# Kernel tuning notes

Hardware: AMD Instinct MI355X
Metric: run time of the kernel (lower is better)

## Reference

```python
import jax, jax.numpy as jnp
import numpy as np

N = 50000      # nodes per graph
E = 600000     # edges per graph
IN_DIM = 512
HID = 128
LAYERS = 2


def setup_inputs() -> dict:
    key = jax.random.key(0)
    ks = jax.random.split(key, 24)
    s = 0.05
    inp = {
        "src_fea": jax.random.normal(ks[0], (N, IN_DIM), jnp.float32),
        "trg_fea": jax.random.normal(ks[1], (N, IN_DIM), jnp.float32),
        "src_row": jax.random.randint(ks[2], (E,), 0, N, jnp.int32),
        "src_col": jax.random.randint(ks[3], (E,), 0, N, jnp.int32),
        "trg_row": jax.random.randint(ks[4], (E,), 0, N, jnp.int32),
        "trg_col": jax.random.randint(ks[5], (E,), 0, N, jnp.int32),
        # fx: Linear(in,hid)+GELU+Linear(hid,hid)+GELU
        "fxW1": jax.random.normal(ks[6], (IN_DIM, HID), jnp.float32) * s,
        "fxb1": jnp.zeros((HID,), jnp.float32),
        "fxW2": jax.random.normal(ks[7], (HID, HID), jnp.float32) * s,
        "fxb2": jnp.zeros((HID,), jnp.float32),
        # edge_att_mlp: Linear(2h,20)+ReLU+Linear(20,10)+ReLU+Linear(10,1)+ReLU
        "eaW1": jax.random.normal(ks[8], (2 * HID, 20), jnp.float32) * s,
        "eab1": jnp.zeros((20,), jnp.float32),
        "eaW2": jax.random.normal(ks[9], (20, 10), jnp.float32) * s,
        "eab2": jnp.zeros((10,), jnp.float32),
        "eaW3": jax.random.normal(ks[10], (10, 1), jnp.float32) * s,
        "eab3": jnp.zeros((1,), jnp.float32),
        # GraphConv (PyG-style, bias=False): out = x@Wroot + agg@Wrel
        "convWroot": jax.random.normal(ks[11], (LAYERS, HID, HID), jnp.float32) * s,
        "convWrel": jax.random.normal(ks[12], (LAYERS, HID, HID), jnp.float32) * s,
    }
    return inp


def _fx(x, W1, b1, W2, b2):
    h = jax.nn.gelu(x @ W1 + b1, approximate=False)
    return jax.nn.gelu(h @ W2 + b2, approximate=False)


def _edge_att(e, eaW1, eab1, eaW2, eab2, eaW3, eab3):
    h = jax.nn.relu(e @ eaW1 + eab1)
    h = jax.nn.relu(h @ eaW2 + eab2)
    h = jax.nn.relu(h @ eaW3 + eab3)
    return jax.nn.sigmoid(h)  # [E,1]


def _graph_conv(x, row, col, ew, Wroot, Wrel):
    # message from source (row) gathered, weighted, aggregated at target (col)
    msg = ew[:, None] * x[row]                                  # [E,h]
    agg = jax.ops.segment_sum(msg, col, num_segments=N)         # [N,h]
    return x @ Wroot + agg @ Wrel


def _branch(x0, row, col, convWroot, convWrel, eaW1, eab1, eaW2, eab2, eaW3, eab3, hard):
    xs, cfds = [], []
    x = x0
    for i in range(LAYERS):
        edge_rep = jnp.concatenate([x[row], x[col]], axis=-1)    # [E,2h]
        att = _edge_att(edge_rep, eaW1, eab1, eaW2, eab2, eaW3, eab3)[:, 0]
        wc = (att + hard) * 0.5
        wo = 1.0 - wc
        x = jax.nn.soft_sign(_graph_conv(x, row, col, wc, convWroot[i], convWrel[i]))
        cfd = jax.nn.soft_sign(_graph_conv(x, row, col, wo, convWroot[i], convWrel[i]))
        xs.append(x)
        cfds.append(cfd)
    return xs, cfds


def reference(src_fea, trg_fea, src_row, src_col, trg_row, trg_col,
              fxW1, fxb1, fxW2, fxb2,
              eaW1, eab1, eaW2, eab2, eaW3, eab3,
              convWroot, convWrel):
    src1 = _fx(src_fea, fxW1, fxb1, fxW2, fxb2)
    trg1 = _fx(trg_fea, fxW1, fxb1, fxW2, fxb2)
    ea = (eaW1, eab1, eaW2, eab2, eaW3, eab3)
    xs_s, cf_s = _branch(src1, src_row, src_col, convWroot, convWrel, *ea, 0.0)
    xs_t, cf_t = _branch(trg1, trg_row, trg_col, convWroot, convWrel, *ea, 0.0)
    # stack: [src1, xs_s..., trg1, xs_t..., cf_s..., cf_t...] -> [2+2*LAYERS+2*LAYERS? no: 10, N, h]
    return jnp.stack([src1] + xs_s + [trg1] + xs_t + cf_s + cf_t, axis=0)
```

## Files before the change

### kernel.cpp

```cpp
#include <hip/hip_runtime.h>
#include <math.h>
#include <stdint.h>


typedef __attribute__((ext_vector_type(8))) short bh8;
typedef __attribute__((ext_vector_type(4))) float f4;

__device__ __forceinline__ float relu_f(float x) { return x > 0.f ? x : 0.f; }

__device__ __forceinline__ unsigned short f2bf(float f) {
    union { float f; unsigned u; } v; v.f = f;
    unsigned r = v.u + 0x7FFF + ((v.u >> 16) & 1);
    return (unsigned short)(r >> 16);
}
__device__ __forceinline__ float bf2f(unsigned short b) {
    union { unsigned u; float f; } v; v.u = ((unsigned)b) << 16;
    return v.f;
}

template<int ACT>
__device__ __forceinline__ float act_fn(float x) {
    if (ACT == 1) return 0.5f * x * (1.f + erff(x * 0.70710678118654752f));
    if (ACT == 2) return x / (1.f + fabsf(x));
    return x;
}

__device__ __forceinline__ void emit_p_phase(short* As, short* Bs,
                                             const short* __restrict__ W56,
                                             short* __restrict__ P,
                                             int row0, int M, int t)
{
    #pragma unroll
    for (int p = 0; p < 4; ++p) {
        int idx = t + 256 * p;
        int r = idx >> 4;
        int c = (idx & 15) * 8;
        *(bh8*)&Bs[r * 136 + c] = *(const bh8*)(W56 + r * 128 + c);
    }
    __syncthreads();
    const int lane = t & 63, w = t >> 6, l15 = lane & 15, l4 = lane >> 4;
    f4 accP[4];
    #pragma unroll
    for (int ni = 0; ni < 4; ++ni) accP[ni] = (f4){0.f, 0.f, 0.f, 0.f};
    #pragma unroll
    for (int kk = 0; kk < 4; ++kk) {
        bh8 a = *(const bh8*)&As[(w * 16 + l15) * 136 + kk * 32 + l4 * 8];
        #pragma unroll
        for (int ni = 0; ni < 4; ++ni) {
            bh8 b = *(const bh8*)&Bs[(ni * 16 + l15) * 136 + kk * 32 + l4 * 8];
            accP[ni] = __builtin_amdgcn_mfma_f32_16x16x32_bf16(a, b, accP[ni], 0, 0, 0);
        }
    }
    #pragma unroll
    for (int ni = 0; ni < 4; ++ni) {
        int col = ni * 16 + l15;
        #pragma unroll
        for (int r = 0; r < 4; ++r) {
            int row = row0 + w * 16 + l4 * 4 + r;
            if (row < M) P[(size_t)row * 64 + col] = (short)f2bf(accP[ni][r]);
        }
    }
}

template<int K, int AF, int ACT, bool BIAS, bool WF32, bool WB16, bool EMITP>
__global__ __launch_bounds__(256, 2)
void mfma_gemm(const void* __restrict__ X0a, const void* __restrict__ X0b,
               const short* __restrict__ W0t, const float* __restrict__ bias,
               float* __restrict__ outfA, short* __restrict__ outbA,
               float* __restrict__ outfB, short* __restrict__ outbB,
               const short* __restrict__ W56,
               short* __restrict__ PA, short* __restrict__ PB, int M)
{
    constexpr int BK  = 64;
    constexpr int LDA = EMITP ? 136 : 72;
    __shared__ short As[64 * LDA];
    __shared__ short Bs[128 * 72];

    const int half = gridDim.x >> 1;
    int bid = blockIdx.x;
    const int g1 = bid >= half;
    bid -= g1 ? half : 0;
    const void* X0v = g1 ? X0b : X0a;
    float* outf = g1 ? outfB : outfA;
    short* outb = g1 ? outbB : outbA;
    short* P    = g1 ? PB : PA;

    const int t    = threadIdx.x;
    const int row0 = bid * 64;
    const int lane = t & 63;
    const int w    = t >> 6;
    const int wr   = w & 1;
    const int wc   = w >> 1;
    const int l15  = lane & 15;
    const int l4   = lane >> 4;

    f4 acc[2][4];
    #pragma unroll
    for (int i = 0; i < 2; ++i)
        #pragma unroll
        for (int j = 0; j < 4; ++j)
            acc[i][j] = (f4){0.f, 0.f, 0.f, 0.f};

    const int ar = t >> 3;
    const int ac = (t & 7) * 8;

    #pragma unroll 1
    for (int k0 = 0; k0 < K; k0 += BK) {
        __syncthreads();
        #pragma unroll
        for (int p = 0; p < 2; ++p) {
            int r    = ar + p * 32;
            int grow = row0 + r;
            bh8 sv = {0, 0, 0, 0, 0, 0, 0, 0};
            if (AF == 0) {
                if (grow < M) {
                    const float* src = (const float*)X0v + (size_t)grow * K + k0 + ac;
                    float4 v0 = *(const float4*)src;
                    float4 v1 = *(const float4*)(src + 4);
                    sv[0] = (short)f2bf(v0.x); sv[1] = (short)f2bf(v0.y);
                    sv[2] = (short)f2bf(v0.z); sv[3] = (short)f2bf(v0.w);
                    sv[4] = (short)f2bf(v1.x); sv[5] = (short)f2bf(v1.y);
                    sv[6] = (short)f2bf(v1.z); sv[7] = (short)f2bf(v1.w);
                }
            } else {
                if (grow < M)
                    sv = *(const bh8*)((const short*)X0v + (size_t)grow * K + k0 + ac);
            }
            *(bh8*)&As[r * LDA + ac] = sv;
        }
        #pragma unroll
        for (int p = 0; p < 4; ++p) {
            int r = ar + p * 32;
            *(bh8*)&Bs[r * 72 + ac] = *(const bh8*)(W0t + (size_t)r * K + k0 + ac);
        }
        __syncthreads();
        #pragma unroll
        for (int kk = 0; kk < 2; ++kk) {
            bh8 a[2], b[4];
            #pragma unroll
            for (int mi = 0; mi < 2; ++mi)
                a[mi] = *(const bh8*)&As[(wr*32 + mi*16 + l15) * LDA + kk*32 + l4*8];
            #pragma unroll
            for (int ni = 0; ni < 4; ++ni)
                b[ni] = *(const bh8*)&Bs[(wc*64 + ni*16 + l15) * 72 + kk*32 + l4*8];
            #pragma unroll
            for (int mi = 0; mi < 2; ++mi)
                #pragma unroll
                for (int ni = 0; ni < 4; ++ni)
                    acc[mi][ni] = __builtin_amdgcn_mfma_f32_16x16x32_bf16(
                        a[mi], b[ni], acc[mi][ni], 0, 0, 0);
        }
    }

    if (EMITP) __syncthreads();
    #pragma unroll
    for (int mi = 0; mi < 2; ++mi) {
        #pragma unroll
        for (int ni = 0; ni < 4; ++ni) {
            int col = wc * 64 + ni * 16 + l15;
            float bv = BIAS ? bias[col] : 0.f;
            #pragma unroll
            for (int r = 0; r < 4; ++r) {
                int rloc = wr * 32 + mi * 16 + l4 * 4 + r;
                int row  = row0 + rloc;
                float v = act_fn<ACT>(acc[mi][ni][r] + bv);
                unsigned short bb = f2bf(v);
                if (row < M) {
                    if (WF32) outf[(size_t)row * 128 + col] = v;
                    if (WB16) outb[(size_t)row * 128 + col] = (short)bb;
                }
                if (EMITP) As[rloc * LDA + col] = (short)bb;
            }
        }
    }
    if (EMITP) emit_p_phase(As, Bs, W56, P, row0, M, t);
}

template<int MODE, bool WB16, bool EMITP>
__global__ __launch_bounds__(256, 2)
void conv_fused(const short* __restrict__ XbA, const short* __restrict__ XbB,
                const int* __restrict__ coffA, const int* __restrict__ coffB,
                const int* __restrict__ crowA, const int* __restrict__ crowB,
                const float* __restrict__ attcA, const float* __restrict__ attcB,
                const short* __restrict__ Wroot, const short* __restrict__ Wrel,
                const short* __restrict__ W56,
                float* __restrict__ outfA, float* __restrict__ outfB,
                short* __restrict__ outbA, short* __restrict__ outbB,
                short* __restrict__ PA, short* __restrict__ PB, int M)
{
    constexpr int LDA = 136;
    __shared__ short As[64 * LDA];
    __shared__ short Bs[128 * 72];

    const int half = gridDim.x >> 1;
    int bid = blockIdx.x;
    const int g1 = bid >= half;
    bid -= g1 ? half : 0;
    const short* Xb   = g1 ? XbB   : XbA;
    const int*   coff = g1 ? coffB : coffA;
    const int*   crow = g1 ? crowB : crowA;
    const float* attc = g1 ? attcB : attcA;
    float* outf = g1 ? outfB : outfA;
    short* outb = g1 ? outbB : outbA;
    short* P    = g1 ? PB : PA;

    const int t    = threadIdx.x;
    const int row0 = bid * 64;
    const int lane = t & 63;
    const int w    = t >> 6;
    const int wr   = w & 1;
    const int wc   = w >> 1;
    const int l15  = lane & 15;
    const int l4   = lane >> 4;

    {
        const int g  = t >> 4;
        const int li = t & 15;
        #pragma unroll 1
        for (int q = 0; q < 4; ++q) {
            int rloc = g * 4 + q;
            int n = row0 + rloc;
            float a8[8] = {0.f, 0.f, 0.f, 0.f, 0.f, 0.f, 0.f, 0.f};
            if (n < M) {
                int p  = coff[n];
                int pe = coff[n + 1];
                for (; p + 7 < pe; p += 8) {
                    float w0 = attc[p],     w1 = attc[p + 1];
                    float w2 = attc[p + 2], w3 = attc[p + 3];
                    float w4 = attc[p + 4], w5 = attc[p + 5];
                    float w6 = attc[p + 6], w7 = attc[p + 7];
                    int r0 = crow[p],     r1 = crow[p + 1];
                    int r2 = crow[p + 2], r3 = crow[p + 3];
                    int r4 = crow[p + 4], r5 = crow[p + 5];
                    int r6 = crow[p + 6], r7 = crow[p + 7];
                    w0 = MODE ? fmaf(-0.5f, w0, 1.f) : 0.5f * w0;
                    w1 = MODE ? fmaf(-0.5f, w1, 1.f) : 0.5f * w1;
                    w2 = MODE ? fmaf(-0.5f, w2, 1.f) : 0.5f * w2;
                    w3 = MODE ? fmaf(-0.5f, w3, 1.f) : 0.5f * w3;
                    w4 = MODE ? fmaf(-0.5f, w4, 1.f) : 0.5f * w4;
                    w5 = MODE ? fmaf(-0.5f, w5, 1.f) : 0.5f * w5;
                    w6 = MODE ? fmaf(-0.5f, w6, 1.f) : 0.5f * w6;
                    w7 = MODE ? fmaf(-0.5f, w7, 1.f) : 0.5f * w7;
                    bh8 v0 = *(const bh8*)&Xb[(size_t)r0 * 128 + li * 8];
                    bh8 v1 = *(const bh8*)&Xb[(size_t)r1 * 128 + li * 8];
                    bh8 v2 = *(const bh8*)&Xb[(size_t)r2 * 128 + li * 8];
                    bh8 v3 = *(const bh8*)&Xb[(size_t)r3 * 128 + li * 8];
                    bh8 v4 = *(const bh8*)&Xb[(size_t)r4 * 128 + li * 8];
                    bh8 v5 = *(const bh8*)&Xb[(size_t)r5 * 128 + li * 8];
                    bh8 v6 = *(const bh8*)&Xb[(size_t)r6 * 128 + li * 8];
                    bh8 v7 = *(const bh8*)&Xb[(size_t)r7 * 128 + li * 8];
                    #pragma unroll
                    for (int j = 0; j < 8; ++j) {
                        a8[j] = fmaf(w0, bf2f((unsigned short)v0[j]), a8[j]);
                        a8[j] = fmaf(w1, bf2f((unsigned short)v1[j]), a8[j]);
                        a8[j] = fmaf(w2, bf2f((unsigned short)v2[j]), a8[j]);
                        a8[j] = fmaf(w3, bf2f((unsigned short)v3[j]), a8[j]);
                        a8[j] = fmaf(w4, bf2f((unsigned short)v4[j]), a8[j]);
                        a8[j] = fmaf(w5, bf2f((unsigned short)v5[j]), a8[j]);
                        a8[j] = fmaf(w6, bf2f((unsigned short)v6[j]), a8[j]);
                        a8[j] = fmaf(w7, bf2f((unsigned short)v7[j]), a8[j]);
                    }
                }
                for (; p + 3 < pe; p += 4) {
                    float w0 = attc[p],     w1 = attc[p + 1];
                    float w2 = attc[p + 2], w3 = attc[p + 3];
                    int r0 = crow[p],     r1 = crow[p + 1];
                    int r2 = crow[p + 2], r3 = crow[p + 3];
                    w0 = MODE ? fmaf(-0.5f, w0, 1.f) : 0.5f * w0;
                    w1 = MODE ? fmaf(-0.5f, w1, 1.f) : 0.5f * w1;
                    w2 = MODE ? fmaf(-0.5f, w2, 1.f) : 0.5f * w2;
                    w3 = MODE ? fmaf(-0.5f, w3, 1.f) : 0.5f * w3;
                    bh8 v0 = *(const bh8*)&Xb[(size_t)r0 * 128 + li * 8];
                    bh8 v1 = *(const bh8*)&Xb[(size_t)r1 * 128 + li * 8];
                    bh8 v2 = *(const bh8*)&Xb[(size_t)r2 * 128 + li * 8];
                    bh8 v3 = *(const bh8*)&Xb[(size_t)r3 * 128 + li * 8];
                    #pragma unroll
                    for (int j = 0; j < 8; ++j) {
                        a8[j] = fmaf(w0, bf2f((unsigned short)v0[j]), a8[j]);
                        a8[j] = fmaf(w1, bf2f((unsigned short)v1[j]), a8[j]);
                        a8[j] = fmaf(w2, bf2f((unsigned short)v2[j]), a8[j]);
                        a8[j] = fmaf(w3, bf2f((unsigned short)v3[j]), a8[j]);
                    }
                }
                for (; p < pe; ++p) {
                    float w0 = attc[p];
                    int   r0 = crow[p];
                    w0 = MODE ? fmaf(-0.5f, w0, 1.f) : 0.5f * w0;
                    bh8 v0 = *(const bh8*)&Xb[(size_t)r0 * 128 + li * 8];
                    #pragma unroll
                    for (int j = 0; j < 8; ++j)
                        a8[j] = fmaf(w0, bf2f((unsigned short)v0[j]), a8[j]);
                }
            }
            bh8 o;
            #pragma unroll
            for (int j = 0; j < 8; ++j) o[j] = (short)f2bf(a8[j]);
            *(bh8*)&As[rloc * LDA + li * 8] = o;
        }
    }
    __syncthreads();

    f4 acc[2][4];
    #pragma unroll
    for (int i = 0; i < 2; ++i)
        #pragma unroll
        for (int j = 0; j < 4; ++j)
            acc[i][j] = (f4){0.f, 0.f, 0.f, 0.f};

    const int ar = t >> 3;
    const int ac = (t & 7) * 8;

    #pragma unroll 1
    for (int k0 = 0; k0 < 128; k0 += 64) {
        if (k0) __syncthreads();
        #pragma unroll
        for (int p = 0; p < 4; ++p) {
            int r = ar + p * 32;
            *(bh8*)&Bs[r * 72 + ac] = *(const bh8*)(Wrel + (size_t)r * 128 + k0 + ac);
        }
        __syncthreads();
        #pragma unroll
        for (int kk = 0; kk < 2; ++kk) {
            bh8 a[2], b[4];
            #pragma unroll
            for (int mi = 0; mi < 2; ++mi)
                a[mi] = *(const bh8*)&As[(wr*32 + mi*16 + l15) * LDA + k0 + kk*32 + l4*8];
            #pragma unroll
            for (int ni = 0; ni < 4; ++ni)
                b[ni] = *(const bh8*)&Bs[(wc*64 + ni*16 + l15) * 72 + kk*32 + l4*8];
            #pragma unroll
            for (int mi = 0; mi < 2; ++mi)
                #pragma unroll
                for (int ni = 0; ni < 4; ++ni)
                    acc[mi][ni] = __builtin_amdgcn_mfma_f32_16x16x32_bf16(
                        a[mi], b[ni], acc[mi][ni], 0, 0, 0);
        }
    }

    #pragma unroll 1
    for (int k0 = 0; k0 < 128; k0 += 64) {
        __syncthreads();
        #pragma unroll
        for (int p = 0; p < 2; ++p) {
            int r    = ar + p * 32;
            int grow = row0 + r;
            bh8 sv = {0, 0, 0, 0, 0, 0, 0, 0};
            if (grow < M)
                sv = *(const bh8*)(Xb + (size_t)grow * 128 + k0 + ac);
            *(bh8*)&As[r * LDA + ac] = sv;
        }
        #pragma unroll
        for (int p = 0; p < 4; ++p) {
            int r = ar + p * 32;
            *(bh8*)&Bs[r * 72 + ac] = *(const bh8*)(Wroot + (size_t)r * 128 + k0 + ac);
        }
        __syncthreads();
        #pragma unroll
        for (int kk = 0; kk < 2; ++kk) {
            bh8 a[2], b[4];
            #pragma unroll
            for (int mi = 0; mi < 2; ++mi)
                a[mi] = *(const bh8*)&As[(wr*32 + mi*16 + l15) * LDA + kk*32 + l4*8];
            #pragma unroll
            for (int ni = 0; ni < 4; ++ni)
                b[ni] = *(const bh8*)&Bs[(wc*64 + ni*16 + l15) * 72 + kk*32 + l4*8];
            #pragma unroll
            for (int mi = 0; mi < 2; ++mi)
                #pragma unroll
                for (int ni = 0; ni < 4; ++ni)
                    acc[mi][ni] = __builtin_amdgcn_mfma_f32_16x16x32_bf16(
                        a[mi], b[ni], acc[mi][ni], 0, 0, 0);
        }
    }

    if (EMITP) __syncthreads();
    #pragma unroll
    for (int mi = 0; mi < 2; ++mi) {
        #pragma unroll
        for (int ni = 0; ni < 4; ++ni) {
            int col = wc * 64 + ni * 16 + l15;
            #pragma unroll
            for (int r = 0; r < 4; ++r) {
                int rloc = wr * 32 + mi * 16 + l4 * 4 + r;
                int row  = row0 + rloc;
                float v = act_fn<2>(acc[mi][ni][r]);
                unsigned short bb = f2bf(v);
                if (row < M) {
                    outf[(size_t)row * 128 + col] = v;
                    if (WB16) outb[(size_t)row * 128 + col] = (short)bb;
                }
                if (EMITP) As[rloc * LDA + col] = (short)bb;
            }
        }
    }
    if (EMITP) emit_p_phase(As, Bs, W56, P, row0, M, t);
}

__global__ void prep_all(const float* __restrict__ eaW1, const float* __restrict__ fxW1,
                         const float* __restrict__ fxW2, const float* __restrict__ convWroot,
                         const float* __restrict__ convWrel,
                         short* __restrict__ w56, short* __restrict__ fxW1t,
                         short* __restrict__ fxW2t, short* __restrict__ wrt,
                         short* __restrict__ wlt)
{
    int i = blockIdx.x * 256 + threadIdx.x;
    if (i < 64 * 128) {
        int j = i >> 7, k = i & 127;
        float v = 0.f;
        if (j < 20)                  v = eaW1[k * 20 + j];
        else if (j >= 32 && j < 52)  v = eaW1[(128 + k) * 20 + (j - 32)];
        w56[i] = (short)f2bf(v);
        return;
    }
    i -= 64 * 128;
    if (i < 512 * 128) {
        int k = i >> 7, n = i & 127;
        fxW1t[(size_t)n * 512 + k] = (short)f2bf(fxW1[i]);
        return;
    }
    i -= 512 * 128;
    if (i < 128 * 128) {
        int k = i >> 7, n = i & 127;
        fxW2t[n * 128 + k] = (short)f2bf(fxW2[i]);
        return;
    }
    i -= 128 * 128;
    if (i < 2 * 128 * 128) {
        int L = i >> 14, r = i & 16383;
        int k = r >> 7, n = r & 127;
        wrt[L * 16384 + n * 128 + k] = (short)f2bf(convWroot[i]);
        return;
    }
    i -= 2 * 128 * 128;
    if (i < 2 * 128 * 128) {
        int L = i >> 14, r = i & 16383;
        int k = r >> 7, n = r & 127;
        wlt[L * 16384 + n * 128 + k] = (short)f2bf(convWrel[i]);
    }
}

__global__ __launch_bounds__(256)
void edge_att_both(const short* __restrict__ PS, const short* __restrict__ PT,
                   const int* __restrict__ rowS, const int* __restrict__ colS,
                   const int* __restrict__ rowT, const int* __restrict__ colT,
                   const int* __restrict__ eposS, const int* __restrict__ eposT,
                   const float* __restrict__ eab1, const float* __restrict__ eaW2,
                   const float* __restrict__ eab2, const float* __restrict__ eaW3,
                   const float* __restrict__ eab3,
                   float* __restrict__ attcS, float* __restrict__ attcT, int E)
{
    __shared__ float w2[200], b2s[10], w3s[10], sb1[20], sb3;
    int t = threadIdx.x;
    if (t < 200) w2[t] = eaW2[t];
    if (t < 20)  sb1[t] = eab1[t];
    if (t < 10)  { b2s[t] = eab2[t]; w3s[t] = eaW3[t]; }
    if (t == 0)  sb3 = eab3[0];
    __syncthreads();

    int idx = blockIdx.x * 256 + t;
    if (idx >= 2 * E) return;
    const int g1 = idx >= E;
    const int e  = idx - (g1 ? E : 0);
    const short* P    = g1 ? PT : PS;
    const int*   row  = g1 ? rowT : rowS;
    const int*   col  = g1 ? colT : colS;
    const int*   epos = g1 ? eposT : eposS;
    float*       attc = g1 ? attcT : attcS;

    int r = row[e], c = col[e];
    const unsigned short* p1 = (const unsigned short*)P + (size_t)r * 64;
    const unsigned short* p2 = (const unsigned short*)P + (size_t)c * 64 + 32;

    bh8 a0 = *(const bh8*)&p1[0];
    bh8 a1 = *(const bh8*)&p1[8];
    ushort4 a2 = *(const ushort4*)&p1[16];
    bh8 b0 = *(const bh8*)&p2[0];
    bh8 b1 = *(const bh8*)&p2[8];
    ushort4 b2 = *(const ushort4*)&p2[16];

    float h1[20];
    #pragma unroll
    for (int j = 0; j < 8; ++j)
        h1[j] = relu_f(bf2f((unsigned short)a0[j]) + bf2f((unsigned short)b0[j]) + sb1[j]);
    #pragma unroll
    for (int j = 0; j < 8; ++j)
        h1[8 + j] = relu_f(bf2f((unsigned short)a1[j]) + bf2f((unsigned short)b1[j]) + sb1[8 + j]);
    h1[16] = relu_f(bf2f(a2.x) + bf2f(b2.x) + sb1[16]);
    h1[17] = relu_f(bf2f(a2.y) + bf2f(b2.y) + sb1[17]);
    h1[18] = relu_f(bf2f(a2.z) + bf2f(b2.z) + sb1[18]);
    h1[19] = relu_f(bf2f(a2.w) + bf2f(b2.w) + sb1[19]);

    float h3 = sb3;
    #pragma unroll
    for (int j2 = 0; j2 < 10; ++j2) {
        float s = b2s[j2];
        #pragma unroll
        for (int j = 0; j < 20; ++j)
            s = fmaf(h1[j], w2[j * 10 + j2], s);
        h3 = fmaf(relu_f(s), w3s[j2], h3);
    }
    h3 = relu_f(h3);
    attc[epos[e]] = 1.f / (1.f + expf(-h3));
}

__global__ void hist_both(const int* __restrict__ colS, const int* __restrict__ colT,
                          int* __restrict__ deg, int N, int E)
{
    int idx = blockIdx.x * 256 + threadIdx.x;
    if (idx >= 2 * E) return;
    const int g1 = idx >= E;
    const int e  = idx - (g1 ? E : 0);
    int c = (g1 ? colT : colS)[e];
    atomicAdd(&deg[(size_t)g1 * N + c], 1);
}

__device__ __forceinline__ int block_incl_scan(int v, int* wsum)
{
    int lane = threadIdx.x & 63;
    int w    = threadIdx.x >> 6;
    #pragma unroll
    for (int off = 1; off < 64; off <<= 1) {
        int t = __shfl_up(v, off);
        if (lane >= off) v += t;
    }
    if (lane == 63) wsum[w] = v;
    __syncthreads();
    int add = 0;
    for (int j = 0; j < w; ++j) add += wsum[j];
    return v + add;
}

__global__ __launch_bounds__(256)
void scanA_both(const int* __restrict__ deg, int* __restrict__ coffS,
                int* __restrict__ coffT, int* __restrict__ bsum, int N)
{
    __shared__ int wsum[4];
    int gy = blockIdx.y;
    const int* d = deg + (size_t)gy * N;
    int* coff    = gy ? coffT : coffS;
    int* bs      = bsum + gy * 256;
    int i = blockIdx.x * 256 + threadIdx.x;
    int orig = (i < N) ? d[i] : 0;
    int v = block_incl_scan(orig, wsum);
    if (i < N) coff[i] = v - orig;
    if (threadIdx.x == 255) bs[blockIdx.x] = v;
}

__global__ __launch_bounds__(256)
void scanB_both(const int* __restrict__ bsum, int* __restrict__ boff, int nb)
{
    __shared__ int wsum[4];
    int gy = blockIdx.y;
    const int* bs = bsum + gy * 256;
    int* bo       = boff + gy * 256;
    int tid = threadIdx.x;
    int orig = (tid < nb) ? bs[tid] : 0;
    int v = block_incl_scan(orig, wsum);
    if (tid < nb) bo[tid] = v - orig;
}

__global__ __launch_bounds__(256)
void scanC_both(int* __restrict__ coffS, int* __restrict__ coffT,
                const int* __restrict__ boff, int* __restrict__ curS,
                int* __restrict__ curT, int N, int E)
{
    int gy = blockIdx.y;
    int* coff = gy ? coffT : coffS;
    int* cur  = gy ? curT  : curS;
    const int* bo = boff + gy * 256;
    int i = blockIdx.x * 256 + threadIdx.x;
    if (i < N) {
        int v = coff[i] + bo[i >> 8];
        coff[i] = v;
        cur[i]  = v;
    }
    if (i == 0) coff[N] = E;
}

__global__ __launch_bounds__(256)
void fill_both(const int* __restrict__ rowS, const int* __restrict__ colS,
               const int* __restrict__ rowT, const int* __restrict__ colT,
               int* __restrict__ curS, int* __restrict__ curT,
               int* __restrict__ crowS, int* __restrict__ crowT,
               int* __restrict__ eposS, int* __restrict__ eposT, int E)
{
    int idx = blockIdx.x * 256 + threadIdx.x;
    if (idx >= 2 * E) return;
    const int g1 = idx >= E;
    const int e  = idx - (g1 ? E : 0);
    const int* row = g1 ? rowT : rowS;
    const int* col = g1 ? colT : colS;
    int* cur  = g1 ? curT  : curS;
    int* crow = g1 ? crowT : crowS;
    int* epos = g1 ? eposT : eposS;
    int c = col[e];
    int p = atomicAdd(&cur[c], 1);
    crow[p] = row[e];
    epos[e] = p;
}


extern "C" void kernel_launch(void* const* d_in, const int* in_sizes, int n_in,
                              void* d_out, int out_size, void* d_ws, size_t ws_size,
                              hipStream_t stream)
{
    const float* src_fea = (const float*)d_in[0];
    const float* trg_fea = (const float*)d_in[1];
    const int*   src_row = (const int*)d_in[2];
    const int*   src_col = (const int*)d_in[3];
    const int*   trg_row = (const int*)d_in[4];
    const int*   trg_col = (const int*)d_in[5];
    const float* fxW1 = (const float*)d_in[6];
    const float* fxb1 = (const float*)d_in[7];
    const float* fxW2 = (const float*)d_in[8];
    const float* fxb2 = (const float*)d_in[9];
    const float* eaW1 = (const float*)d_in[10];
    const float* eab1 = (const float*)d_in[11];
    const float* eaW2 = (const float*)d_in[12];
    const float* eab2 = (const float*)d_in[13];
    const float* eaW3 = (const float*)d_in[14];
    const float* eab3 = (const float*)d_in[15];
    const float* convWroot = (const float*)d_in[16];
    const float* convWrel  = (const float*)d_in[17];

    const int N = in_sizes[0] / 512;
    const int E = in_sizes[2];

    float* out = (float*)d_out;
    const size_t slot_sz = (size_t)N * 128;
    auto slot = [&](int i) { return out + (size_t)i * slot_sz; };

    float* fp    = (float*)d_ws;
    float* attcS = fp; fp += E;
    float* attcT = fp; fp += E;
    int* ip    = (int*)fp;
    int* deg   = ip; ip += 2 * N;
    int* bsum  = ip; ip += 512;
    int* boff  = ip; ip += 512;
    int* coffS = ip; ip += N + 2;
    int* coffT = ip; ip += N + 2;
    int* curS  = ip; ip += N;
    int* curT  = ip; ip += N;
    int* crowS = ip; ip += E;
    int* crowT = ip; ip += E;
    int* eposS = ip; ip += E;
    int* eposT = ip; ip += E;
    short* sp = (short*)((((uintptr_t)ip) + 255) & ~(uintptr_t)255);
    short* xb0   = sp; sp += slot_sz;
    short* xb1   = sp; sp += slot_sz;
    short* xsbS[2]; short* xsbT[2];
    xsbS[0] = sp; sp += slot_sz;
    xsbS[1] = sp; sp += slot_sz;
    xsbT[0] = sp; sp += slot_sz;
    xsbT[1] = sp; sp += slot_sz;
    short* PS    = sp; sp += (size_t)N * 64;
    short* PT    = sp; sp += (size_t)N * 64;
    short* w56   = sp; sp += 64 * 128;
    short* fxW1t = sp; sp += 128 * 512;
    short* fxW2t = sp; sp += 128 * 128;
    short* wrt   = sp; sp += 2 * 128 * 128;
    short* wlt   = sp; sp += 2 * 128 * 128;

    const int prep_total = 64*128 + 512*128 + 128*128 + 2*128*128 + 2*128*128;
    prep_all<<<(prep_total + 255) / 256, 256, 0, stream>>>(
        eaW1, fxW1, fxW2, convWroot, convWrel, w56, fxW1t, fxW2t, wrt, wlt);

    const int gb = (N + 63) / 64;
    short* hS = xsbS[0];
    short* hT = xsbT[0];
    mfma_gemm<512, 0, 1, true, false, true, false><<<2 * gb, 256, 0, stream>>>(
        src_fea, trg_fea, fxW1t, fxb1,
        nullptr, hS, nullptr, hT, nullptr, nullptr, nullptr, N);
    mfma_gemm<128, 1, 1, true, true, true, true><<<2 * gb, 256, 0, stream>>>(
        hS, hT, fxW2t, fxb2,
        slot(0), xb0, slot(3), xb1, w56, PS, PT, N);

    const int e2grid  = (2 * E + 255) / 256;
    const int nchunks = (N + 255) / 256;
    hipMemsetAsync(deg, 0, (size_t)2 * N * sizeof(int), stream);
    hist_both<<<e2grid, 256, 0, stream>>>(src_col, trg_col, deg, N, E);
    scanA_both<<<dim3(nchunks, 2), 256, 0, stream>>>(deg, coffS, coffT, bsum, N);
    scanB_both<<<dim3(1, 2), 256, 0, stream>>>(bsum, boff, nchunks);
    scanC_both<<<dim3(nchunks, 2), 256, 0, stream>>>(coffS, coffT, boff, curS, curT, N, E);
    fill_both<<<e2grid, 256, 0, stream>>>(src_row, src_col, trg_row, trg_col,
                                          curS, curT, crowS, crowT, eposS, eposT, E);

    short* xbS = xb0;
    short* xbT = xb1;
    for (int L = 0; L < 2; ++L) {
        float* xs_s = slot(1 + L);
        float* xs_t = slot(4 + L);
        float* cf_s = slot(6 + L);
        float* cf_t = slot(8 + L);
        const short* WrT = wrt + (size_t)L * 16384;
        const short* WlT = wlt + (size_t)L * 16384;

        edge_att_both<<<e2grid, 256, 0, stream>>>(PS, PT, src_row, src_col,
            trg_row, trg_col, eposS, eposT, eab1, eaW2, eab2, eaW3, eab3,
            attcS, attcT, E);

        if (L == 0)
            conv_fused<0, true, true><<<2 * gb, 256, 0, stream>>>(
                xbS, xbT, coffS, coffT, crowS, crowT, attcS, attcT,
                WrT, WlT, w56, xs_s, xs_t, xsbS[L], xsbT[L], PS, PT, N);
        else
            conv_fused<0, true, false><<<2 * gb, 256, 0, stream>>>(
                xbS, xbT, coffS, coffT, crowS, crowT, attcS, attcT,
                WrT, WlT, nullptr, xs_s, xs_t, xsbS[L], xsbT[L], nullptr, nullptr, N);

        conv_fused<1, false, false><<<2 * gb, 256, 0, stream>>>(
            xsbS[L], xsbT[L], coffS, coffT, crowS, crowT, attcS, attcT,
            WrT, WlT, nullptr, cf_s, cf_t, nullptr, nullptr, nullptr, nullptr, N);

        xbS = xsbS[L];
        xbT = xsbT[L];
    }
}
```

Before: 641.8 us.

## Fuse degree histogram into prep kernel and layer-0 edge attention into CSR fill

Merges the edge-degree histogram into the weight-prep launch by giving that kernel extra blocks, which removes one launch and lets the histogram run before the fx GEMMs. The layer-0 edge-attention MLP is moved into the CSR fill kernel: each edge is already read there, so the row/col loads and one full edge pass are shared. The separate edge_att launch now runs only for layer 1. This removes two kernel launches and one edge pass, but the fill kernel now carries more registers and scattered P loads alongside its atomics.

```diff
diff --git a/kernel.cpp b/kernel.cpp
--- a/kernel.cpp
+++ b/kernel.cpp
@@ -23,6 +23,44 @@
     if (ACT == 1) return 0.5f * x * (1.f + erff(x * 0.70710678118654752f));
     if (ACT == 2) return x / (1.f + fabsf(x));
     return x;
+}
+
+__device__ __forceinline__ float edge_att_mlp(const unsigned short* p1,
+                                              const unsigned short* p2,
+                                              const float* w2, const float* b2s,
+                                              const float* w3s, const float* sb1,
+                                              float sb3)
+{
+    bh8 a0 = *(const bh8*)&p1[0];
+    bh8 a1 = *(const bh8*)&p1[8];
+    ushort4 a2 = *(const ushort4*)&p1[16];
+    bh8 b0 = *(const bh8*)&p2[0];
+    bh8 b1 = *(const bh8*)&p2[8];
+    ushort4 b2 = *(const ushort4*)&p2[16];
+
+    float h1[20];
+    #pragma unroll
+    for (int j = 0; j < 8; ++j)
+        h1[j] = relu_f(bf2f((unsigned short)a0[j]) + bf2f((unsigned short)b0[j]) + sb1[j]);
+    #pragma unroll
+    for (int j = 0; j < 8; ++j)
+        h1[8 + j] = relu_f(bf2f((unsigned short)a1[j]) + bf2f((unsigned short)b1[j]) + sb1[8 + j]);
+    h1[16] = relu_f(bf2f(a2.x) + bf2f(b2.x) + sb1[16]);
+    h1[17] = relu_f(bf2f(a2.y) + bf2f(b2.y) + sb1[17]);
+    h1[18] = relu_f(bf2f(a2.z) + bf2f(b2.z) + sb1[18]);
+    h1[19] = relu_f(bf2f(a2.w) + bf2f(b2.w) + sb1[19]);
+
+    float h3 = sb3;
+    #pragma unroll
+    for (int j2 = 0; j2 < 10; ++j2) {
+        float s = b2s[j2];
+        #pragma unroll
+        for (int j = 0; j < 20; ++j)
+            s = fmaf(h1[j], w2[j * 10 + j2], s);
+        h3 = fmaf(relu_f(s), w3s[j2], h3);
+    }
+    h3 = relu_f(h3);
+    return 1.f / (1.f + expf(-h3));
 }
 
 __device__ __forceinline__ void emit_p_phase(short* As, short* Bs,
@@ -396,13 +434,24 @@
     if (EMITP) emit_p_phase(As, Bs, W56, P, row0, M, t);
 }
 
-__global__ void prep_all(const float* __restrict__ eaW1, const float* __restrict__ fxW1,
-                         const float* __restrict__ fxW2, const float* __restrict__ convWroot,
-                         const float* __restrict__ convWrel,
-                         short* __restrict__ w56, short* __restrict__ fxW1t,
-                         short* __restrict__ fxW2t, short* __restrict__ wrt,
-                         short* __restrict__ wlt)
-{
+__global__ void prep_hist(const float* __restrict__ eaW1, const float* __restrict__ fxW1,
+                          const float* __restrict__ fxW2, const float* __restrict__ convWroot,
+                          const float* __restrict__ convWrel,
+                          short* __restrict__ w56, short* __restrict__ fxW1t,
+                          short* __restrict__ fxW2t, short* __restrict__ wrt,
+                          short* __restrict__ wlt,
+                          const int* __restrict__ colS, const int* __restrict__ colT,
+                          int* __restrict__ deg, int N, int E, int prepBlocks)
+{
+    if ((int)blockIdx.x >= prepBlocks) {
+        int idx = (blockIdx.x - prepBlocks) * 256 + threadIdx.x;
+        if (idx >= 2 * E) return;
+        const int g1 = idx >= E;
+        const int e  = idx - (g1 ? E : 0);
+        int c = (g1 ? colT : colS)[e];
+        atomicAdd(&deg[(size_t)g1 * N + c], 1);
+        return;
+    }
     int i = blockIdx.x * 256 + threadIdx.x;
     if (i < 64 * 128) {
         int j = i >> 7, k = i & 127;
@@ -470,48 +519,7 @@
     int r = row[e], c = col[e];
     const unsigned short* p1 = (const unsigned short*)P + (size_t)r * 64;
     const unsigned short* p2 = (const unsigned short*)P + (size_t)c * 64 + 32;
-
-    bh8 a0 = *(const bh8*)&p1[0];
-    bh8 a1 = *(const bh8*)&p1[8];
-    ushort4 a2 = *(const ushort4*)&p1[16];
-    bh8 b0 = *(const bh8*)&p2[0];
-    bh8 b1 = *(const bh8*)&p2[8];
-    ushort4 b2 = *(const ushort4*)&p2[16];
-
-    float h1[20];
-    #pragma unroll
-    for (int j = 0; j < 8; ++j)
-        h1[j] = relu_f(bf2f((unsigned short)a0[j]) + bf2f((unsigned short)b0[j]) + sb1[j]);
-    #pragma unroll
-    for (int j = 0; j < 8; ++j)
-        h1[8 + j] = relu_f(bf2f((unsigned short)a1[j]) + bf2f((unsigned short)b1[j]) + sb1[8 + j]);
-    h1[16] = relu_f(bf2f(a2.x) + bf2f(b2.x) + sb1[16]);
-    h1[17] = relu_f(bf2f(a2.y) + bf2f(b2.y) + sb1[17]);
-    h1[18] = relu_f(bf2f(a2.z) + bf2f(b2.z) + sb1[18]);
-    h1[19] = relu_f(bf2f(a2.w) + bf2f(b2.w) + sb1[19]);
-
-    float h3 = sb3;
-    #pragma unroll
-    for (int j2 = 0; j2 < 10; ++j2) {
-        float s = b2s[j2];
-        #pragma unroll
-        for (int j = 0; j < 20; ++j)
-            s = fmaf(h1[j], w2[j * 10 + j2], s);
-        h3 = fmaf(relu_f(s), w3s[j2], h3);
-    }
-    h3 = relu_f(h3);
-    attc[epos[e]] = 1.f / (1.f + expf(-h3));
-}
-
-__global__ void hist_both(const int* __restrict__ colS, const int* __restrict__ colT,
-                          int* __restrict__ deg, int N, int E)
-{
-    int idx = blockIdx.x * 256 + threadIdx.x;
-    if (idx >= 2 * E) return;
-    const int g1 = idx >= E;
-    const int e  = idx - (g1 ? E : 0);
-    int c = (g1 ? colT : colS)[e];
-    atomicAdd(&deg[(size_t)g1 * N + c], 1);
+    attc[epos[e]] = edge_att_mlp(p1, p2, w2, b2s, w3s, sb1, sb3);
 }
 
 __device__ __forceinline__ int block_incl_scan(int v, int* wsum)
@@ -578,13 +586,26 @@
 }
 
 __global__ __launch_bounds__(256)
-void fill_both(const int* __restrict__ rowS, const int* __restrict__ colS,
-               const int* __restrict__ rowT, const int* __restrict__ colT,
-               int* __restrict__ curS, int* __restrict__ curT,
-               int* __restrict__ crowS, int* __restrict__ crowT,
-               int* __restrict__ eposS, int* __restrict__ eposT, int E)
-{
-    int idx = blockIdx.x * 256 + threadIdx.x;
+void fill_att_both(const int* __restrict__ rowS, const int* __restrict__ colS,
+                   const int* __restrict__ rowT, const int* __restrict__ colT,
+                   int* __restrict__ curS, int* __restrict__ curT,
+                   int* __restrict__ crowS, int* __restrict__ crowT,
+                   int* __restrict__ eposS, int* __restrict__ eposT,
+                   const short* __restrict__ PS, const short* __restrict__ PT,
+                   const float* __restrict__ eab1, const float* __restrict__ eaW2,
+                   const float* __restrict__ eab2, const float* __restrict__ eaW3,
+                   const float* __restrict__ eab3,
+                   float* __restrict__ attcS, float* __restrict__ attcT, int E)
+{
+    __shared__ float w2[200], b2s[10], w3s[10], sb1[20], sb3;
+    int t = threadIdx.x;
+    if (t < 200) w2[t] = eaW2[t];
+    if (t < 20)  sb1[t] = eab1[t];
+    if (t < 10)  { b2s[t] = eab2[t]; w3s[t] = eaW3[t]; }
+    if (t == 0)  sb3 = eab3[0];
+    __syncthreads();
+
+    int idx = blockIdx.x * 256 + t;
     if (idx >= 2 * E) return;
     const int g1 = idx >= E;
     const int e  = idx - (g1 ? E : 0);
@@ -593,10 +614,18 @@
     int* cur  = g1 ? curT  : curS;
     int* crow = g1 ? crowT : crowS;
     int* epos = g1 ? eposT : eposS;
+    const short* P = g1 ? PT : PS;
+    float* attc    = g1 ? attcT : attcS;
+
     int c = col[e];
+    int r = row[e];
     int p = atomicAdd(&cur[c], 1);
-    crow[p] = row[e];
+    crow[p] = r;
     epos[e] = p;
+
+    const unsigned short* p1 = (const unsigned short*)P + (size_t)r * 64;
+    const unsigned short* p2 = (const unsigned short*)P + (size_t)c * 64 + 32;
+    attc[p] = edge_att_mlp(p1, p2, w2, b2s, w3s, sb1, sb3);
 }
 
 
@@ -661,9 +690,15 @@
     short* wrt   = sp; sp += 2 * 128 * 128;
     short* wlt   = sp; sp += 2 * 128 * 128;
 
+    const int e2grid  = (2 * E + 255) / 256;
+    const int nchunks = (N + 255) / 256;
+
+    hipMemsetAsync(deg, 0, (size_t)2 * N * sizeof(int), stream);
     const int prep_total = 64*128 + 512*128 + 128*128 + 2*128*128 + 2*128*128;
-    prep_all<<<(prep_total + 255) / 256, 256, 0, stream>>>(
-        eaW1, fxW1, fxW2, convWroot, convWrel, w56, fxW1t, fxW2t, wrt, wlt);
+    const int prepBlocks = (prep_total + 255) / 256;
+    prep_hist<<<prepBlocks + e2grid, 256, 0, stream>>>(
+        eaW1, fxW1, fxW2, convWroot, convWrel, w56, fxW1t, fxW2t, wrt, wlt,
+        src_col, trg_col, deg, N, E, prepBlocks);
 
     const int gb = (N + 63) / 64;
     short* hS = xsbS[0];
@@ -675,15 +710,12 @@
         hS, hT, fxW2t, fxb2,
         slot(0), xb0, slot(3), xb1, w56, PS, PT, N);
 
-    const int e2grid  = (2 * E + 255) / 256;
-    const int nchunks = (N + 255) / 256;
-    hipMemsetAsync(deg, 0, (size_t)2 * N * sizeof(int), stream);
-    hist_both<<<e2grid, 256, 0, stream>>>(src_col, trg_col, deg, N, E);
     scanA_both<<<dim3(nchunks, 2), 256, 0, stream>>>(deg, coffS, coffT, bsum, N);
     scanB_both<<<dim3(1, 2), 256, 0, stream>>>(bsum, boff, nchunks);
     scanC_both<<<dim3(nchunks, 2), 256, 0, stream>>>(coffS, coffT, boff, curS, curT, N, E);
-    fill_both<<<e2grid, 256, 0, stream>>>(src_row, src_col, trg_row, trg_col,
-                                          curS, curT, crowS, crowT, eposS, eposT, E);
+    fill_att_both<<<e2grid, 256, 0, stream>>>(
+        src_row, src_col, trg_row, trg_col, curS, curT, crowS, crowT,
+        eposS, eposT, PS, PT, eab1, eaW2, eab2, eaW3, eab3, attcS, attcT, E);
 
     short* xbS = xb0;
     short* xbT = xb1;
@@ -695,9 +727,10 @@
         const short* WrT = wrt + (size_t)L * 16384;
         const short* WlT = wlt + (size_t)L * 16384;
 
-        edge_att_both<<<e2grid, 256, 0, stream>>>(PS, PT, src_row, src_col,
-            trg_row, trg_col, eposS, eposT, eab1, eaW2, eab2, eaW3, eab3,
-            attcS, attcT, E);
+        if (L == 1)
+            edge_att_both<<<e2grid, 256, 0, stream>>>(PS, PT, src_row, src_col,
+                trg_row, trg_col, eposS, eposT, eab1, eaW2, eab2, eaW3, eab3,
+                attcS, attcT, E);
 
         if (L == 0)
             conv_fused<0, true, true><<<2 * gb, 256, 0, stream>>>(
```

New measurement: 594.3 us. 1.08x faster.
